# Kernel optimization log

Measured on AMD Instinct MI355X. Metric: run time of the kernel, lower is better.

The kernel has to match this reference:

```python
import jax, jax.numpy as jnp
import numpy as np

NQ, NL, PD, B = 4, 2, 64, 524288
RANGES = [1, 2]  # StronglyEntanglingLayers default: (l % (nq-1)) + 1


def setup_inputs() -> dict:
    key = jax.random.key(0)
    ks = jax.random.split(key, 4)
    x = jax.random.normal(ks[0], (B, NQ), jnp.float32)
    # PennyLane TorchLayer default init: uniform [0, 2pi)
    weights = jax.random.uniform(ks[1], (NL, NQ, 3), jnp.float32, 0.0, 2.0 * np.pi)
    W = jax.random.normal(ks[2], (PD, NQ), jnp.float32) / np.sqrt(NQ)
    b = jnp.zeros((PD,), jnp.float32)
    gamma = jnp.ones((PD,), jnp.float32)
    beta = jnp.zeros((PD,), jnp.float32)
    return {"x": x, "weights": weights, "W": W, "b": b, "gamma": gamma, "beta": beta}


def _apply_1q_batched(state, gate, w):
    # state: [B, 2,2,2,2], gate: [B,2,2], act on wire w (axis w+1)
    s = jnp.moveaxis(state, w + 1, -1)
    s = jnp.einsum('bij,b...j->b...i', gate, s)
    return jnp.moveaxis(s, -1, w + 1)


def _apply_1q_shared(state, gate, w):
    s = jnp.moveaxis(state, w + 1, -1)
    s = jnp.einsum('ij,b...j->b...i', gate, s)
    return jnp.moveaxis(s, -1, w + 1)


def _cnot(state, c, t):
    s = jnp.moveaxis(state, (c + 1, t + 1), (-2, -1))
    s = jnp.stack([s[..., 0, :], s[..., 1, ::-1]], axis=-2)  # flip target where control=1
    return jnp.moveaxis(s, (-2, -1), (c + 1, t + 1))


def _rot(phi, theta, omega):
    # Rot = RZ(omega) RY(theta) RZ(phi)
    ct, st = jnp.cos(theta / 2), jnp.sin(theta / 2)
    ep = jnp.exp(-0.5j * (phi + omega))
    em = jnp.exp(-0.5j * (phi - omega))
    return jnp.array([[ep * ct, -jnp.conj(em) * st],
                      [em * st, jnp.conj(ep) * ct]])


def _circuit(x, weights):
    n = x.shape[0]
    state = jnp.zeros((n,) + (2,) * NQ, jnp.complex64)
    state = state.at[(slice(None),) + (0,) * NQ].set(1.0)
    # AngleEmbedding (RX rotations)
    half = x * 0.5
    c, s = jnp.cos(half), jnp.sin(half)
    for w in range(NQ):
        cw, sw = c[:, w], -1j * s[:, w]
        g = jnp.stack([jnp.stack([cw + 0j, sw], -1),
                       jnp.stack([sw, cw + 0j], -1)], -2)  # [B,2,2]
        state = _apply_1q_batched(state, g, w)
    # StronglyEntanglingLayers
    for l in range(NL):
        for w in range(NQ):
            state = _apply_1q_shared(state, _rot(weights[l, w, 0], weights[l, w, 1], weights[l, w, 2]), w)
        r = RANGES[l]
        for w in range(NQ):
            state = _cnot(state, w, (w + r) % NQ)
    probs = state.real ** 2 + state.imag ** 2  # [B,2,2,2,2]
    zs = []
    for w in range(NQ):
        other = tuple(a for a in range(1, NQ + 1) if a != w + 1)
        m = probs.sum(other)  # [B,2]
        zs.append(m[:, 0] - m[:, 1])  # <Z_w>
    return jnp.stack(zs, -1)  # [B,4]


def reference(x, weights, W, b, gamma, beta):
    xt = jnp.tanh(x) * jnp.pi
    q = _circuit(xt, weights)
    q = jax.nn.softmax(q, axis=-1)
    h = q @ W.T + b  # [B, 64]
    mu = h.mean(-1, keepdims=True)
    var = ((h - mu) ** 2).mean(-1, keepdims=True)
    return (h - mu) / jnp.sqrt(var + 1e-5) * gamma + beta
```

## Files before the change

kernel.cpp:

```cpp
#include <hip/hip_runtime.h>

#define BLK 256
#define PD 64
#define PI_F 3.14159265358979323846f

__device__ __forceinline__ float fast_tanh(float v) {
    float e = __expf(2.0f * v);
    return 1.0f - 2.0f / (e + 1.0f);
}

template<int M>
__device__ __forceinline__ void gate_apply(float* ar, float* ai,
        float u00r, float u00i, float u01r, float u01i,
        float u10r, float u10i, float u11r, float u11i) {
    #pragma unroll
    for (int i = 0; i < 16; ++i) {
        if (i & M) continue;
        const int j = i | M;
        const float a0r = ar[i], a0i = ai[i], a1r = ar[j], a1i = ai[j];
        ar[i] = u00r*a0r - u00i*a0i + u01r*a1r - u01i*a1i;
        ai[i] = u00r*a0i + u00i*a0r + u01r*a1i + u01i*a1r;
        ar[j] = u10r*a0r - u10i*a0i + u11r*a1r - u11i*a1i;
        ai[j] = u10r*a0i + u10i*a0r + u11r*a1i + u11i*a1r;
    }
}

template<int CM, int TM>
__device__ __forceinline__ void cnotg(float* ar, float* ai) {
    #pragma unroll
    for (int i = 0; i < 16; ++i) {
        if ((i & CM) && !(i & TM)) {
            const int j = i | TM;
            float tp;
            tp = ar[i]; ar[i] = ar[j]; ar[j] = tp;
            tp = ai[i]; ai[i] = ai[j]; ai[j] = tp;
        }
    }
}

extern "C" __global__ void __launch_bounds__(64)
qbranch_prep(const float* __restrict__ wts, const float* __restrict__ W,
             const float* __restrict__ bias, float* __restrict__ ws)
{
    const int t = threadIdx.x;
    const float4 wr = reinterpret_cast<const float4*>(W)[t];
    const float bp = bias[t];
    float v[20] = { wr.x*wr.x, wr.x*wr.y, wr.x*wr.z, wr.x*wr.w,
                    wr.y*wr.y, wr.y*wr.z, wr.y*wr.w,
                    wr.z*wr.z, wr.z*wr.w,
                    wr.w*wr.w,
                    wr.x*bp, wr.y*bp, wr.z*bp, wr.w*bp,
                    wr.x, wr.y, wr.z, wr.w,
                    bp, bp*bp };
    #pragma unroll
    for (int o = 32; o > 0; o >>= 1) {
        #pragma unroll
        for (int k = 0; k < 20; ++k) v[k] += __shfl_xor(v[k], o, 64);
    }
    if (t == 0) {
        #pragma unroll
        for (int k = 0; k < 20; ++k) ws[64 + k] = v[k] * (1.0f / 64.0f);
    }
    if (t < 8) {
        const float phi = wts[t * 3 + 0];
        const float th  = wts[t * 3 + 1];
        const float om  = wts[t * 3 + 2];
        float st, ct;  __sincosf(0.5f * th, &st, &ct);
        float sa, ca;  __sincosf(0.5f * (phi + om), &sa, &ca);
        float sb, cb;  __sincosf(0.5f * (phi - om), &sb, &cb);
        float* gg = ws + t * 8;
        gg[0] =  ct * ca;  gg[1] = -ct * sa;
        gg[2] = -st * cb;  gg[3] = -st * sb;
        gg[4] =  st * cb;  gg[5] = -st * sb;
        gg[6] =  ct * ca;  gg[7] =  ct * sa;
    }
}

extern "C" __global__ void __launch_bounds__(BLK)
qbranch_main(const float* __restrict__ x,
             const float* __restrict__ W,
             const float* __restrict__ bias,
             const float* __restrict__ gamma,
             const float* __restrict__ beta,
             const float* __restrict__ cw,
             float* __restrict__ out)
{
    __shared__ float4 sq4[BLK];
    __shared__ float2 sms[BLK];

    const int t = threadIdx.x;
    const int b = blockIdx.x * BLK + t;
    const float4 xv = reinterpret_cast<const float4*>(x)[b];

    float v0r[4], v0i[4], v1r[4], v1i[4];
    const float xs[4] = {xv.x, xv.y, xv.z, xv.w};
    #pragma unroll
    for (int w = 0; w < 4; ++w) {
        float s, c;
        __sincosf(0.5f * PI_F * fast_tanh(xs[w]), &s, &c);
        const float g0 = cw[w*8+0], g1 = cw[w*8+1], g2 = cw[w*8+2], g3 = cw[w*8+3];
        const float g4 = cw[w*8+4], g5 = cw[w*8+5], g6 = cw[w*8+6], g7 = cw[w*8+7];
        v0r[w] = fmaf(c, g0,  s * g3);
        v0i[w] = fmaf(c, g1, -s * g2);
        v1r[w] = fmaf(c, g4,  s * g7);
        v1i[w] = fmaf(c, g5, -s * g6);
    }

    float Ar[4], Ai[4], Br[4], Bi[4];
    #pragma unroll
    for (int j = 0; j < 4; ++j) {
        const int b0 = j >> 1, b1 = j & 1;
        const float p0r = b0 ? v1r[0] : v0r[0], p0i = b0 ? v1i[0] : v0i[0];
        const float p1r = b1 ? v1r[1] : v0r[1], p1i = b1 ? v1i[1] : v0i[1];
        Ar[j] = p0r*p1r - p0i*p1i;
        Ai[j] = p0r*p1i + p0i*p1r;
        const float p2r = b0 ? v1r[2] : v0r[2], p2i = b0 ? v1i[2] : v0i[2];
        const float p3r = b1 ? v1r[3] : v0r[3], p3i = b1 ? v1i[3] : v0i[3];
        Br[j] = p2r*p3r - p2i*p3i;
        Bi[j] = p2r*p3i + p2i*p3r;
    }
    float ar[16], ai[16];
    #pragma unroll
    for (int i = 0; i < 16; ++i) {
        const int hi = i >> 2, lo = i & 3;
        ar[i] = Ar[hi]*Br[lo] - Ai[hi]*Bi[lo];
        ai[i] = Ar[hi]*Bi[lo] + Ai[hi]*Br[lo];
    }

    cnotg<8, 4>(ar, ai);
    cnotg<4, 2>(ar, ai);
    cnotg<2, 1>(ar, ai);
    cnotg<1, 8>(ar, ai);

    gate_apply<8>(ar, ai, cw[32], cw[33], cw[34], cw[35], cw[36], cw[37], cw[38], cw[39]);
    gate_apply<4>(ar, ai, cw[40], cw[41], cw[42], cw[43], cw[44], cw[45], cw[46], cw[47]);
    gate_apply<2>(ar, ai, cw[48], cw[49], cw[50], cw[51], cw[52], cw[53], cw[54], cw[55]);
    gate_apply<1>(ar, ai, cw[56], cw[57], cw[58], cw[59], cw[60], cw[61], cw[62], cw[63]);

    cnotg<8, 2>(ar, ai);
    cnotg<4, 1>(ar, ai);
    cnotg<2, 8>(ar, ai);
    cnotg<1, 4>(ar, ai);

    float z0 = 0.f, z1 = 0.f, z2 = 0.f, z3 = 0.f;
    #pragma unroll
    for (int i = 0; i < 16; ++i) {
        const float p = ar[i]*ar[i] + ai[i]*ai[i];
        z0 += (i & 8) ? -p : p;
        z1 += (i & 4) ? -p : p;
        z2 += (i & 2) ? -p : p;
        z3 += (i & 1) ? -p : p;
    }
    const float mx = fmaxf(fmaxf(z0, z1), fmaxf(z2, z3));
    const float e0 = __expf(z0 - mx), e1 = __expf(z1 - mx);
    const float e2 = __expf(z2 - mx), e3 = __expf(z3 - mx);
    const float inv = 1.0f / (e0 + e1 + e2 + e3);
    const float q0 = e0 * inv, q1 = e1 * inv, q2 = e2 * inv, q3 = e3 * inv;

    const float* sS = cw + 64;
    const float mu = fmaf(q0, sS[14], fmaf(q1, sS[15], fmaf(q2, sS[16], fmaf(q3, sS[17], sS[18]))));
    const float t0 = sS[0]*q0 + sS[1]*q1 + sS[2]*q2 + sS[3]*q3 + 2.0f*sS[10];
    const float t1 = sS[1]*q0 + sS[4]*q1 + sS[5]*q2 + sS[6]*q3 + 2.0f*sS[11];
    const float t2 = sS[2]*q0 + sS[5]*q1 + sS[7]*q2 + sS[8]*q3 + 2.0f*sS[12];
    const float t3 = sS[3]*q0 + sS[6]*q1 + sS[8]*q2 + sS[9]*q3 + 2.0f*sS[13];
    const float Eh2 = t0*q0 + t1*q1 + t2*q2 + t3*q3 + sS[19];
    const float rstd = rsqrtf(Eh2 - mu * mu + 1e-5f);

    sq4[t] = make_float4(q0, q1, q2, q3);
    sms[t] = make_float2(mu, rstd);

    const int p4 = t & 15;
    const float4 w0 = reinterpret_cast<const float4*>(W)[p4 * 4 + 0];
    const float4 w1 = reinterpret_cast<const float4*>(W)[p4 * 4 + 1];
    const float4 w2 = reinterpret_cast<const float4*>(W)[p4 * 4 + 2];
    const float4 w3 = reinterpret_cast<const float4*>(W)[p4 * 4 + 3];
    const float4 bg = reinterpret_cast<const float4*>(bias)[p4];
    const float4 gm = reinterpret_cast<const float4*>(gamma)[p4];
    const float4 bt = reinterpret_cast<const float4*>(beta)[p4];

    __syncthreads();

    const int sub = t >> 4;
    const size_t base = (size_t)blockIdx.x * (BLK * PD);
    #pragma unroll 4
    for (int it = 0; it < 16; ++it) {
        const int row = it * 16 + sub;
        const float4 qv = sq4[row];
        const float2 ms = sms[row];
        const float h0 = fmaf(qv.x, w0.x, fmaf(qv.y, w0.y, fmaf(qv.z, w0.z, fmaf(qv.w, w0.w, bg.x))));
        const float h1 = fmaf(qv.x, w1.x, fmaf(qv.y, w1.y, fmaf(qv.z, w1.z, fmaf(qv.w, w1.w, bg.y))));
        const float h2 = fmaf(qv.x, w2.x, fmaf(qv.y, w2.y, fmaf(qv.z, w2.z, fmaf(qv.w, w2.w, bg.z))));
        const float h3 = fmaf(qv.x, w3.x, fmaf(qv.y, w3.y, fmaf(qv.z, w3.z, fmaf(qv.w, w3.w, bg.w))));
        float4 pk;
        pk.x = fmaf((h0 - ms.x), ms.y * gm.x, bt.x);
        pk.y = fmaf((h1 - ms.x), ms.y * gm.y, bt.y);
        pk.z = fmaf((h2 - ms.x), ms.y * gm.z, bt.z);
        pk.w = fmaf((h3 - ms.x), ms.y * gm.w, bt.w);
        *reinterpret_cast<float4*>(&out[base + (size_t)row * PD + p4 * 4]) = pk;
    }
}

extern "C" void kernel_launch(void* const* d_in, const int* in_sizes, int n_in,
                              void* d_out, int out_size, void* d_ws, size_t ws_size,
                              hipStream_t stream) {
    const float* x     = (const float*)d_in[0];
    const float* wts   = (const float*)d_in[1];
    const float* W     = (const float*)d_in[2];
    const float* bias  = (const float*)d_in[3];
    const float* gamma = (const float*)d_in[4];
    const float* beta  = (const float*)d_in[5];
    float* ws  = (float*)d_ws;
    float* out = (float*)d_out;
    const int B = in_sizes[0] / 4;
    hipLaunchKernelGGL(qbranch_prep, dim3(1), dim3(64), 0, stream, wts, W, bias, ws);
    hipLaunchKernelGGL(qbranch_main, dim3(B / BLK), dim3(BLK), 0, stream,
                       x, W, bias, gamma, beta, ws, out);
}
```

Baseline: 174.5 us.

## Precompute circuit as trigonometric polynomial tensors, evaluate per sample

The prep kernel now builds the full 4-qubit entangling unitary from the weights and contracts it into 81-coefficient tensors per Z expectation in the basis {1, cos x, sin x} of each embedded angle. The main kernel evaluates these multilinear polynomials instead of simulating the 16-amplitude state vector per sample. This removes the per-sample gate arithmetic but adds 324 uniform coefficient loads and a heavier single-block prep kernel that uses shared atomics. The workspace moves to a device global array.

```diff
diff --git a/kernel.cpp b/kernel.cpp
--- a/kernel.cpp
+++ b/kernel.cpp
@@ -3,6 +3,8 @@
 #define BLK 256
 #define PD 64
 #define PI_F 3.14159265358979323846f
+
+__device__ float g_ws[344];
 
 __device__ __forceinline__ float fast_tanh(float v) {
     float e = __expf(2.0f * v);
@@ -38,28 +40,35 @@
     }
 }
 
-extern "C" __global__ void __launch_bounds__(64)
+extern "C" __global__ void __launch_bounds__(256)
 qbranch_prep(const float* __restrict__ wts, const float* __restrict__ W,
-             const float* __restrict__ bias, float* __restrict__ ws)
+             const float* __restrict__ bias)
 {
+    __shared__ float gL[64];
+    __shared__ float uRe[16][16];
+    __shared__ float uIm[16][16];
+    __shared__ float tL[324];
     const int t = threadIdx.x;
-    const float4 wr = reinterpret_cast<const float4*>(W)[t];
-    const float bp = bias[t];
-    float v[20] = { wr.x*wr.x, wr.x*wr.y, wr.x*wr.z, wr.x*wr.w,
-                    wr.y*wr.y, wr.y*wr.z, wr.y*wr.w,
-                    wr.z*wr.z, wr.z*wr.w,
-                    wr.w*wr.w,
-                    wr.x*bp, wr.y*bp, wr.z*bp, wr.w*bp,
-                    wr.x, wr.y, wr.z, wr.w,
-                    bp, bp*bp };
-    #pragma unroll
-    for (int o = 32; o > 0; o >>= 1) {
-        #pragma unroll
-        for (int k = 0; k < 20; ++k) v[k] += __shfl_xor(v[k], o, 64);
-    }
-    if (t == 0) {
-        #pragma unroll
-        for (int k = 0; k < 20; ++k) ws[64 + k] = v[k] * (1.0f / 64.0f);
+
+    if (t < 64) {
+        const float4 wr = reinterpret_cast<const float4*>(W)[t];
+        const float bp = bias[t];
+        float v[20] = { wr.x*wr.x, wr.x*wr.y, wr.x*wr.z, wr.x*wr.w,
+                        wr.y*wr.y, wr.y*wr.z, wr.y*wr.w,
+                        wr.z*wr.z, wr.z*wr.w,
+                        wr.w*wr.w,
+                        wr.x*bp, wr.y*bp, wr.z*bp, wr.w*bp,
+                        wr.x, wr.y, wr.z, wr.w,
+                        bp, bp*bp };
+        #pragma unroll
+        for (int o = 32; o > 0; o >>= 1) {
+            #pragma unroll
+            for (int k = 0; k < 20; ++k) v[k] += __shfl_xor(v[k], o, 64);
+        }
+        if (t == 0) {
+            #pragma unroll
+            for (int k = 0; k < 20; ++k) g_ws[324 + k] = v[k] * (1.0f / 64.0f);
+        }
     }
     if (t < 8) {
         const float phi = wts[t * 3 + 0];
@@ -68,12 +77,124 @@
         float st, ct;  __sincosf(0.5f * th, &st, &ct);
         float sa, ca;  __sincosf(0.5f * (phi + om), &sa, &ca);
         float sb, cb;  __sincosf(0.5f * (phi - om), &sb, &cb);
-        float* gg = ws + t * 8;
+        float* gg = gL + t * 8;
         gg[0] =  ct * ca;  gg[1] = -ct * sa;
         gg[2] = -st * cb;  gg[3] = -st * sb;
         gg[4] =  st * cb;  gg[5] = -st * sb;
         gg[6] =  ct * ca;  gg[7] =  ct * sa;
     }
+    for (int k = t; k < 324; k += 256) tL[k] = 0.f;
+    __syncthreads();
+
+    if (t < 16) {
+        float v0r[4], v0i[4], v1r[4], v1i[4];
+        #pragma unroll
+        for (int u = 0; u < 4; ++u) {
+            const float* g = gL + u * 8;
+            const int bsel = (t >> (3 - u)) & 1;
+            v0r[u] = bsel ? g[2] : g[0];  v0i[u] = bsel ? g[3] : g[1];
+            v1r[u] = bsel ? g[6] : g[4];  v1i[u] = bsel ? g[7] : g[5];
+        }
+        float Ar[4], Ai[4], Br[4], Bi[4];
+        #pragma unroll
+        for (int j = 0; j < 4; ++j) {
+            const int b0 = j >> 1, b1 = j & 1;
+            const float p0r = b0 ? v1r[0] : v0r[0], p0i = b0 ? v1i[0] : v0i[0];
+            const float p1r = b1 ? v1r[1] : v0r[1], p1i = b1 ? v1i[1] : v0i[1];
+            Ar[j] = p0r*p1r - p0i*p1i;
+            Ai[j] = p0r*p1i + p0i*p1r;
+            const float p2r = b0 ? v1r[2] : v0r[2], p2i = b0 ? v1i[2] : v0i[2];
+            const float p3r = b1 ? v1r[3] : v0r[3], p3i = b1 ? v1i[3] : v0i[3];
+            Br[j] = p2r*p3r - p2i*p3i;
+            Bi[j] = p2r*p3i + p2i*p3r;
+        }
+        float ar[16], ai[16];
+        #pragma unroll
+        for (int i = 0; i < 16; ++i) {
+            const int hi = i >> 2, lo = i & 3;
+            ar[i] = Ar[hi]*Br[lo] - Ai[hi]*Bi[lo];
+            ai[i] = Ar[hi]*Bi[lo] + Ai[hi]*Br[lo];
+        }
+        cnotg<8, 4>(ar, ai);
+        cnotg<4, 2>(ar, ai);
+        cnotg<2, 1>(ar, ai);
+        cnotg<1, 8>(ar, ai);
+        gate_apply<8>(ar, ai, gL[32],gL[33],gL[34],gL[35],gL[36],gL[37],gL[38],gL[39]);
+        gate_apply<4>(ar, ai, gL[40],gL[41],gL[42],gL[43],gL[44],gL[45],gL[46],gL[47]);
+        gate_apply<2>(ar, ai, gL[48],gL[49],gL[50],gL[51],gL[52],gL[53],gL[54],gL[55]);
+        gate_apply<1>(ar, ai, gL[56],gL[57],gL[58],gL[59],gL[60],gL[61],gL[62],gL[63]);
+        cnotg<8, 2>(ar, ai);
+        cnotg<4, 1>(ar, ai);
+        cnotg<2, 8>(ar, ai);
+        cnotg<1, 4>(ar, ai);
+        #pragma unroll
+        for (int m = 0; m < 16; ++m) { uRe[t][m] = ar[m]; uIm[t][m] = ai[m]; }
+    }
+    __syncthreads();
+
+    {
+        const int i = t >> 4, j = t & 15;
+        float pr[16], pq[16];
+        #pragma unroll
+        for (int m = 0; m < 16; ++m) {
+            const float air = uRe[i][m], aii = uIm[i][m];
+            const float ajr = uRe[j][m], aji = uIm[j][m];
+            pr[m] = air*ajr + aii*aji;
+            pq[m] = air*aji - aii*ajr;
+        }
+        float hr[4], hq[4];
+        #pragma unroll
+        for (int w = 0; w < 4; ++w) {
+            float sr = 0.f, si = 0.f;
+            #pragma unroll
+            for (int m = 0; m < 16; ++m) {
+                const float sg = ((m >> (3 - w)) & 1) ? -1.f : 1.f;
+                sr += sg * pr[m];  si += sg * pq[m];
+            }
+            hr[w] = sr; hq[w] = si;
+        }
+        int   tA[4], tB[4];
+        float cAr[4], cAi[4], cBr[4], cBi[4];
+        #pragma unroll
+        for (int u = 0; u < 4; ++u) {
+            const int iu = (i >> (3 - u)) & 1, ju = (j >> (3 - u)) & 1;
+            if (iu == 0 && ju == 0)      { tA[u]=0; cAr[u]=0.5f; cAi[u]=0.f;  tB[u]=1; cBr[u]= 0.5f; cBi[u]=0.f; }
+            else if (iu == 1 && ju == 1) { tA[u]=0; cAr[u]=0.5f; cAi[u]=0.f;  tB[u]=1; cBr[u]=-0.5f; cBi[u]=0.f; }
+            else if (iu == 0 && ju == 1) { tA[u]=2; cAr[u]=0.f;  cAi[u]=-0.5f; tB[u]=2; cBr[u]=0.f;  cBi[u]=0.f; }
+            else                         { tA[u]=2; cAr[u]=0.f;  cAi[u]= 0.5f; tB[u]=2; cBr[u]=0.f;  cBi[u]=0.f; }
+        }
+        #pragma unroll
+        for (int a0 = 0; a0 < 2; ++a0) {
+            const int   x0  = a0 ? tB[0] : tA[0];
+            const float p0r = a0 ? cBr[0] : cAr[0], p0i = a0 ? cBi[0] : cAi[0];
+            #pragma unroll
+            for (int a1 = 0; a1 < 2; ++a1) {
+                const int   x1  = a1 ? tB[1] : tA[1];
+                const float q1r = a1 ? cBr[1] : cAr[1], q1i = a1 ? cBi[1] : cAi[1];
+                const float m1r = p0r*q1r - p0i*q1i, m1i = p0r*q1i + p0i*q1r;
+                #pragma unroll
+                for (int a2 = 0; a2 < 2; ++a2) {
+                    const int   x2  = a2 ? tB[2] : tA[2];
+                    const float q2r = a2 ? cBr[2] : cAr[2], q2i = a2 ? cBi[2] : cAi[2];
+                    const float m2r = m1r*q2r - m1i*q2i, m2i = m1r*q2i + m1i*q2r;
+                    #pragma unroll
+                    for (int a3 = 0; a3 < 2; ++a3) {
+                        const int   x3  = a3 ? tB[3] : tA[3];
+                        const float q3r = a3 ? cBr[3] : cAr[3], q3i = a3 ? cBi[3] : cAi[3];
+                        const float m3r = m2r*q3r - m2i*q3i, m3i = m2r*q3i + m2i*q3r;
+                        const int idx = ((x0*3 + x1)*3 + x2)*3 + x3;
+                        #pragma unroll
+                        for (int w = 0; w < 4; ++w) {
+                            const float contrib = hr[w]*m3r - hq[w]*m3i;
+                            atomicAdd(&tL[w*81 + idx], contrib);
+                        }
+                    }
+                }
+            }
+        }
+    }
+    __syncthreads();
+    for (int k = t; k < 324; k += 256) g_ws[k] = tL[k];
 }
 
 extern "C" __global__ void __launch_bounds__(BLK)
@@ -82,7 +203,6 @@
              const float* __restrict__ bias,
              const float* __restrict__ gamma,
              const float* __restrict__ beta,
-             const float* __restrict__ cw,
              float* __restrict__ out)
 {
     __shared__ float4 sq4[BLK];
@@ -91,79 +211,55 @@
     const int t = threadIdx.x;
     const int b = blockIdx.x * BLK + t;
     const float4 xv = reinterpret_cast<const float4*>(x)[b];
-
-    float v0r[4], v0i[4], v1r[4], v1i[4];
+    const float* cw = g_ws;
+
+    float C[4], S[4];
     const float xs[4] = {xv.x, xv.y, xv.z, xv.w};
     #pragma unroll
+    for (int w = 0; w < 4; ++w)
+        __sincosf(PI_F * fast_tanh(xs[w]), &S[w], &C[w]);
+
+    const float e0v[3] = {1.f, C[0], S[0]};
+    const float e1v[3] = {1.f, C[1], S[1]};
+    const float e2v[3] = {1.f, C[2], S[2]};
+
+    float z[4];
+    #pragma unroll
     for (int w = 0; w < 4; ++w) {
-        float s, c;
-        __sincosf(0.5f * PI_F * fast_tanh(xs[w]), &s, &c);
-        const float g0 = cw[w*8+0], g1 = cw[w*8+1], g2 = cw[w*8+2], g3 = cw[w*8+3];
-        const float g4 = cw[w*8+4], g5 = cw[w*8+5], g6 = cw[w*8+6], g7 = cw[w*8+7];
-        v0r[w] = fmaf(c, g0,  s * g3);
-        v0i[w] = fmaf(c, g1, -s * g2);
-        v1r[w] = fmaf(c, g4,  s * g7);
-        v1i[w] = fmaf(c, g5, -s * g6);
-    }
-
-    float Ar[4], Ai[4], Br[4], Bi[4];
-    #pragma unroll
-    for (int j = 0; j < 4; ++j) {
-        const int b0 = j >> 1, b1 = j & 1;
-        const float p0r = b0 ? v1r[0] : v0r[0], p0i = b0 ? v1i[0] : v0i[0];
-        const float p1r = b1 ? v1r[1] : v0r[1], p1i = b1 ? v1i[1] : v0i[1];
-        Ar[j] = p0r*p1r - p0i*p1i;
-        Ai[j] = p0r*p1i + p0i*p1r;
-        const float p2r = b0 ? v1r[2] : v0r[2], p2i = b0 ? v1i[2] : v0i[2];
-        const float p3r = b1 ? v1r[3] : v0r[3], p3i = b1 ? v1i[3] : v0i[3];
-        Br[j] = p2r*p3r - p2i*p3i;
-        Bi[j] = p2r*p3i + p2i*p3r;
-    }
-    float ar[16], ai[16];
-    #pragma unroll
-    for (int i = 0; i < 16; ++i) {
-        const int hi = i >> 2, lo = i & 3;
-        ar[i] = Ar[hi]*Br[lo] - Ai[hi]*Bi[lo];
-        ai[i] = Ar[hi]*Bi[lo] + Ai[hi]*Br[lo];
-    }
-
-    cnotg<8, 4>(ar, ai);
-    cnotg<4, 2>(ar, ai);
-    cnotg<2, 1>(ar, ai);
-    cnotg<1, 8>(ar, ai);
-
-    gate_apply<8>(ar, ai, cw[32], cw[33], cw[34], cw[35], cw[36], cw[37], cw[38], cw[39]);
-    gate_apply<4>(ar, ai, cw[40], cw[41], cw[42], cw[43], cw[44], cw[45], cw[46], cw[47]);
-    gate_apply<2>(ar, ai, cw[48], cw[49], cw[50], cw[51], cw[52], cw[53], cw[54], cw[55]);
-    gate_apply<1>(ar, ai, cw[56], cw[57], cw[58], cw[59], cw[60], cw[61], cw[62], cw[63]);
-
-    cnotg<8, 2>(ar, ai);
-    cnotg<4, 1>(ar, ai);
-    cnotg<2, 8>(ar, ai);
-    cnotg<1, 4>(ar, ai);
-
-    float z0 = 0.f, z1 = 0.f, z2 = 0.f, z3 = 0.f;
-    #pragma unroll
-    for (int i = 0; i < 16; ++i) {
-        const float p = ar[i]*ar[i] + ai[i]*ai[i];
-        z0 += (i & 8) ? -p : p;
-        z1 += (i & 4) ? -p : p;
-        z2 += (i & 2) ? -p : p;
-        z3 += (i & 1) ? -p : p;
-    }
-    const float mx = fmaxf(fmaxf(z0, z1), fmaxf(z2, z3));
-    const float e0 = __expf(z0 - mx), e1 = __expf(z1 - mx);
-    const float e2 = __expf(z2 - mx), e3 = __expf(z3 - mx);
+        const float* T = cw + w * 81;
+        float acc0 = 0.f;
+        #pragma unroll
+        for (int t0 = 0; t0 < 3; ++t0) {
+            float acc1 = 0.f;
+            #pragma unroll
+            for (int t1 = 0; t1 < 3; ++t1) {
+                float acc2 = 0.f;
+                #pragma unroll
+                for (int t2 = 0; t2 < 3; ++t2) {
+                    const float* Tp = T + (((t0*3) + t1)*3 + t2)*3;
+                    const float r = fmaf(S[3], Tp[2], fmaf(C[3], Tp[1], Tp[0]));
+                    acc2 = fmaf(e2v[t2], r, acc2);
+                }
+                acc1 = fmaf(e1v[t1], acc2, acc1);
+            }
+            acc0 = fmaf(e0v[t0], acc1, acc0);
+        }
+        z[w] = acc0;
+    }
+
+    const float mx = fmaxf(fmaxf(z[0], z[1]), fmaxf(z[2], z[3]));
+    const float e0 = __expf(z[0] - mx), e1 = __expf(z[1] - mx);
+    const float e2 = __expf(z[2] - mx), e3 = __expf(z[3] - mx);
     const float inv = 1.0f / (e0 + e1 + e2 + e3);
     const float q0 = e0 * inv, q1 = e1 * inv, q2 = e2 * inv, q3 = e3 * inv;
 
-    const float* sS = cw + 64;
+    const float* sS = cw + 324;
     const float mu = fmaf(q0, sS[14], fmaf(q1, sS[15], fmaf(q2, sS[16], fmaf(q3, sS[17], sS[18]))));
-    const float t0 = sS[0]*q0 + sS[1]*q1 + sS[2]*q2 + sS[3]*q3 + 2.0f*sS[10];
-    const float t1 = sS[1]*q0 + sS[4]*q1 + sS[5]*q2 + sS[6]*q3 + 2.0f*sS[11];
-    const float t2 = sS[2]*q0 + sS[5]*q1 + sS[7]*q2 + sS[8]*q3 + 2.0f*sS[12];
-    const float t3 = sS[3]*q0 + sS[6]*q1 + sS[8]*q2 + sS[9]*q3 + 2.0f*sS[13];
-    const float Eh2 = t0*q0 + t1*q1 + t2*q2 + t3*q3 + sS[19];
+    const float t0m = sS[0]*q0 + sS[1]*q1 + sS[2]*q2 + sS[3]*q3 + 2.0f*sS[10];
+    const float t1m = sS[1]*q0 + sS[4]*q1 + sS[5]*q2 + sS[6]*q3 + 2.0f*sS[11];
+    const float t2m = sS[2]*q0 + sS[5]*q1 + sS[7]*q2 + sS[8]*q3 + 2.0f*sS[12];
+    const float t3m = sS[3]*q0 + sS[6]*q1 + sS[8]*q2 + sS[9]*q3 + 2.0f*sS[13];
+    const float Eh2 = t0m*q0 + t1m*q1 + t2m*q2 + t3m*q3 + sS[19];
     const float rstd = rsqrtf(Eh2 - mu * mu + 1e-5f);
 
     sq4[t] = make_float4(q0, q1, q2, q3);
@@ -209,10 +305,9 @@
     const float* bias  = (const float*)d_in[3];
     const float* gamma = (const float*)d_in[4];
     const float* beta  = (const float*)d_in[5];
-    float* ws  = (float*)d_ws;
     float* out = (float*)d_out;
     const int B = in_sizes[0] / 4;
-    hipLaunchKernelGGL(qbranch_prep, dim3(1), dim3(64), 0, stream, wts, W, bias, ws);
+    hipLaunchKernelGGL(qbranch_prep, dim3(1), dim3(64 * 4), 0, stream, wts, W, bias);
     hipLaunchKernelGGL(qbranch_main, dim3(B / BLK), dim3(BLK), 0, stream,
-                       x, W, bias, gamma, beta, ws, out);
-}
+                       x, W, bias, gamma, beta, out);
+}
```

Result: slower. 201.3 us (+15.4%).
